# Performance work log

Hardware: AMD Instinct MI355X
Metric: run time of the kernel (lower is better)

The kernel has to match this reference:

```python
import jax, jax.numpy as jnp
import numpy as np

N, IN_F, OUT_F = 65536, 512, 512


def setup_inputs() -> dict:
    key = jax.random.key(0)
    k1, k2, k3 = jax.random.split(key, 3)
    # Activations arrive as dequant-pending uint8-valued floats in [0, 256).
    x = jax.random.randint(k1, (N, IN_F), 0, 256).astype(jnp.float32)
    weight = jax.random.randint(k2, (OUT_F, IN_F), 0, 256).astype(jnp.int32)
    bias = jax.random.randint(k3, (OUT_F,), -512, 512).astype(jnp.int32)
    return {
        "x": x,
        "weight": weight,
        "bias": bias,
        "M": jnp.asarray(0.0123, dtype=jnp.float32),
        "x_zero": jnp.asarray(128.0, dtype=jnp.float32),
        "w_zero": jnp.asarray(128.0, dtype=jnp.float32),
        "y_zero": jnp.asarray(128.0, dtype=jnp.float32),
    }


def reference(x, weight, bias, M, x_zero, w_zero, y_zero):
    # y = round(linear(x - x_zero, w - w_zero, b) * M + y_zero)
    xs = x - x_zero                                   # [N, IN_F]
    w = weight.astype(jnp.float32) - w_zero           # [OUT_F, IN_F]
    y = jnp.einsum("ni,oi->no", xs, w) + bias.astype(jnp.float32)
    return jnp.round(y * M + y_zero)
```

## Files before the change

### kernel.cpp

```cpp
#include <hip/hip_runtime.h>


#define K_DIM 512
#define OUTF  512
#define NT    8

typedef __attribute__((ext_vector_type(4))) int   i32x4;
typedef __attribute__((ext_vector_type(4))) float f32x4;
typedef __attribute__((ext_vector_type(2))) unsigned int u32x2;

__global__ void wprep(const int* __restrict__ W, unsigned int* __restrict__ Wb,
                      const float* __restrict__ wzp) {
    const int wz = __float2int_rn(wzp[0]);
    int idx = (blockIdx.x * blockDim.x + threadIdx.x) * 4;
    i32x4 w = *reinterpret_cast<const i32x4*>(W + idx);
    unsigned int p = ((unsigned int)(w[0] - wz) & 0xffu)
                   | (((unsigned int)(w[1] - wz) & 0xffu) << 8)
                   | (((unsigned int)(w[2] - wz) & 0xffu) << 16)
                   | (((unsigned int)(w[3] - wz) & 0xffu) << 24);
    Wb[idx >> 2] = p;
}

__global__ __launch_bounds__(512, 4)
void qgemm(const float* __restrict__ X,
           const unsigned char* __restrict__ Wb,
           const int* __restrict__ bias,
           const float* __restrict__ Mp,
           const float* __restrict__ xzp,
           const float* __restrict__ yzp,
           float* __restrict__ Y) {
    __shared__ unsigned char lds[2][4096];

    const int tid  = threadIdx.x;
    const int lane = tid & 63;
    const int wid  = tid >> 6;
    const int fr   = lane & 15;
    const int fq   = lane >> 4;

    const int row0 = blockIdx.x * 64;
    const int c0   = wid * 64;

    const float xzf = xzp[0];

    const int srow = tid >> 3;
    const int sk   = (tid & 7) * 8;
    const float* xbase = X + (size_t)(row0 + srow) * K_DIM + sk;
    const int ldst = (srow >> 4) * 1024 + ((srow & 15) + ((sk >> 4) << 4)) * 16 + (sk & 8);

    f32x4 ra[2][2];

    auto stageA = [&](int t, int s) {
        const float* p = xbase + t * 64;
        ra[s][0] = *reinterpret_cast<const f32x4*>(p);
        ra[s][1] = *reinterpret_cast<const f32x4*>(p + 4);
    };
    auto convwrite = [&](int buf, int s) {
        u32x2 v;
        #pragma unroll
        for (int h = 0; h < 2; ++h) {
            unsigned int u0 = (unsigned int)((int)(ra[s][h][0] - xzf)) & 0xffu;
            unsigned int u1 = (unsigned int)((int)(ra[s][h][1] - xzf)) & 0xffu;
            unsigned int u2 = (unsigned int)((int)(ra[s][h][2] - xzf)) & 0xffu;
            unsigned int u3 = (unsigned int)((int)(ra[s][h][3] - xzf)) & 0xffu;
            v[h] = u0 | (u1 << 8) | (u2 << 16) | (u3 << 24);
        }
        *reinterpret_cast<u32x2*>(&lds[buf][ldst]) = v;
    };

    i32x4 acc[4][4];
    #pragma unroll
    for (int n = 0; n < 4; ++n) {
        const int bv = bias[c0 + n * 16 + fr];
        #pragma unroll
        for (int m = 0; m < 4; ++m)
            acc[m][n] = i32x4{bv, bv, bv, bv};
    }

    const unsigned char* wbb = Wb + (size_t)(c0 + fr) * K_DIM + fq * 16;

    auto compute = [&](int buf, int ks) {
        i32x4 af[4], bf[4];
        #pragma unroll
        for (int m = 0; m < 4; ++m)
            af[m] = *reinterpret_cast<const i32x4*>(&lds[buf][m * 1024 + lane * 16]);
        #pragma unroll
        for (int n = 0; n < 4; ++n)
            bf[n] = *reinterpret_cast<const i32x4*>(wbb + (size_t)n * 16 * K_DIM + ks * 64);
        #pragma unroll
        for (int m = 0; m < 4; ++m)
            #pragma unroll
            for (int n = 0; n < 4; ++n)
                acc[m][n] = __builtin_amdgcn_mfma_i32_16x16x64_i8(
                    af[m], bf[n], acc[m][n], 0, 0, 0);
    };

    auto barrier = [&]() {
        asm volatile("s_waitcnt lgkmcnt(0)" ::: "memory");
        __builtin_amdgcn_s_barrier();
    };

    stageA(0, 0);
    stageA(1, 1);
    convwrite(0, 0);
    barrier();

    #pragma unroll
    for (int t = 0; t < NT; ++t) {
        if (t + 2 < NT) stageA(t + 2, t & 1);
        compute(t & 1, t);
        if (t + 1 < NT) convwrite((t + 1) & 1, (t + 1) & 1);
        barrier();
    }

    const float Mv = Mp[0], yz = yzp[0];
    #pragma unroll
    for (int n = 0; n < 4; ++n) {
        const int col = c0 + n * 16 + fr;
        #pragma unroll
        for (int m = 0; m < 4; ++m) {
            const int row = row0 + m * 16 + fq * 4;
            float* yp = Y + (size_t)row * OUTF + col;
            #pragma unroll
            for (int j = 0; j < 4; ++j)
                yp[(size_t)j * OUTF] = rintf((float)acc[m][n][j] * Mv + yz);
        }
    }
}

extern "C" void kernel_launch(void* const* d_in, const int* in_sizes, int n_in,
                              void* d_out, int out_size, void* d_ws, size_t ws_size,
                              hipStream_t stream) {
    const float* x    = (const float*)d_in[0];
    const int*   w    = (const int*)d_in[1];
    const int*   bias = (const int*)d_in[2];
    const float* M    = (const float*)d_in[3];
    const float* xz   = (const float*)d_in[4];
    const float* wz   = (const float*)d_in[5];
    const float* yz   = (const float*)d_in[6];
    float* y = (float*)d_out;

    unsigned int* Wb = (unsigned int*)d_ws;

    wprep<<<256, 256, 0, stream>>>(w, Wb, wz);
    qgemm<<<1024, 512, 0, stream>>>(x, (const unsigned char*)Wb, bias, M, xz, yz, y);
}
```

Baseline: 78.66 us.

## Warp-specialize qgemm into producer/consumer waves with 128x128 tiles and triple buffering

Splits each block into four producer waves and four MFMA consumer waves. The producers convert fp32 X to int8 into LDS and bring weights in with global_load_lds, while the consumers compute from a three-stage LDS ring. Tiles change from 64 rows by all 512 columns to 128x128, with an XCD-aware block remap so the four column tiles of a row band land on the same L2. The aim is to overlap conversion and loads with MFMA work and to serve weights from LDS. The cost is that each X row band is now fetched by four blocks, which adds global or L2 traffic on what is already a bandwidth-bound fp32 input, and half the waves no longer issue MFMAs.

Result: slower. 101.3 us (+28.7%).

```diff
diff --git a/kernel.cpp b/kernel.cpp
--- a/kernel.cpp
+++ b/kernel.cpp
@@ -7,7 +7,12 @@
 
 typedef __attribute__((ext_vector_type(4))) int   i32x4;
 typedef __attribute__((ext_vector_type(4))) float f32x4;
-typedef __attribute__((ext_vector_type(2))) unsigned int u32x2;
+
+__device__ __forceinline__ void gload16(const void* g, void* l) {
+    __builtin_amdgcn_global_load_lds(
+        (const __attribute__((address_space(1))) void*)g,
+        (__attribute__((address_space(3))) void*)l, 16, 0, 0);
+}
 
 __global__ void wprep(const int* __restrict__ W, unsigned int* __restrict__ Wb,
                       const float* __restrict__ wzp) {
@@ -29,100 +34,128 @@
            const float* __restrict__ xzp,
            const float* __restrict__ yzp,
            float* __restrict__ Y) {
-    __shared__ unsigned char lds[2][4096];
+    __shared__ unsigned char lds[3][16384];
 
     const int tid  = threadIdx.x;
     const int lane = tid & 63;
     const int wid  = tid >> 6;
-    const int fr   = lane & 15;
-    const int fq   = lane >> 4;
 
-    const int row0 = blockIdx.x * 64;
-    const int c0   = wid * 64;
+    const int b = blockIdx.x;
+    const int lid = (b & 7) * 256 + (b >> 3);
+    const int row0 = (lid >> 2) * 128;
+    const int n0   = (lid & 3) * 128;
 
-    const float xzf = xzp[0];
+    if (wid < 4) {
+        const float xzf = xzp[0];
+        const int j = tid;
+        const int r = j >> 1;
+        const int mfrag = r >> 4;
+        const int dA = mfrag * 1024 + ((r & 15) + 32 * (j & 1)) * 16;
+        const float* xbase = X + (size_t)(row0 + r) * K_DIM + (j & 1) * 32;
+        const unsigned char* wbase =
+            Wb + (size_t)(n0 + wid * 32 + (lane & 15)) * K_DIM + (lane >> 4) * 16;
 
-    const int srow = tid >> 3;
-    const int sk   = (tid & 7) * 8;
-    const float* xbase = X + (size_t)(row0 + srow) * K_DIM + sk;
-    const int ldst = (srow >> 4) * 1024 + ((srow & 15) + ((sk >> 4) << 4)) * 16 + (sk & 8);
+        f32x4 ra[2][8];
 
-    f32x4 ra[2][2];
+        auto stageA = [&](int tt) {
+            const float* p = xbase + tt * 64;
+            #pragma unroll
+            for (int q = 0; q < 8; ++q)
+                ra[tt & 1][q] = *reinterpret_cast<const f32x4*>(p + q * 4);
+        };
+        auto gloadB = [&](int tt) {
+            unsigned char* base = &lds[tt % 3][8192 + (2 * wid) * 1024];
+            const unsigned char* g = wbase + tt * 64;
+            gload16(g,              base);
+            gload16(g + 16 * K_DIM, base + 1024);
+        };
+        auto convwrite = [&](int tt) {
+            int pk[8];
+            #pragma unroll
+            for (int w = 0; w < 8; ++w) {
+                const f32x4 v = ra[tt & 1][w];
+                unsigned int u0 = (unsigned int)((int)(v[0] - xzf)) & 0xffu;
+                unsigned int u1 = (unsigned int)((int)(v[1] - xzf)) & 0xffu;
+                unsigned int u2 = (unsigned int)((int)(v[2] - xzf)) & 0xffu;
+                unsigned int u3 = (unsigned int)((int)(v[3] - xzf)) & 0xffu;
+                pk[w] = (int)(u0 | (u1 << 8) | (u2 << 16) | (u3 << 24));
+            }
+            unsigned char* base = &lds[tt % 3][dA];
+            *reinterpret_cast<i32x4*>(base)       = i32x4{pk[0], pk[1], pk[2], pk[3]};
+            *reinterpret_cast<i32x4*>(base + 256) = i32x4{pk[4], pk[5], pk[6], pk[7]};
+        };
 
-    auto stageA = [&](int t, int s) {
-        const float* p = xbase + t * 64;
-        ra[s][0] = *reinterpret_cast<const f32x4*>(p);
-        ra[s][1] = *reinterpret_cast<const f32x4*>(p + 4);
-    };
-    auto convwrite = [&](int buf, int s) {
-        u32x2 v;
+        stageA(0); gloadB(0); stageA(1); gloadB(1);
+        convwrite(0);
+        __builtin_amdgcn_sched_barrier(0);
+        asm volatile("s_waitcnt vmcnt(10) lgkmcnt(0)" ::: "memory");
+        __builtin_amdgcn_s_barrier();
+
         #pragma unroll
-        for (int h = 0; h < 2; ++h) {
-            unsigned int u0 = (unsigned int)((int)(ra[s][h][0] - xzf)) & 0xffu;
-            unsigned int u1 = (unsigned int)((int)(ra[s][h][1] - xzf)) & 0xffu;
-            unsigned int u2 = (unsigned int)((int)(ra[s][h][2] - xzf)) & 0xffu;
-            unsigned int u3 = (unsigned int)((int)(ra[s][h][3] - xzf)) & 0xffu;
-            v[h] = u0 | (u1 << 8) | (u2 << 16) | (u3 << 24);
+        for (int t = 0; t < NT - 2; ++t) {
+            stageA(t + 2);
+            gloadB(t + 2);
+            convwrite(t + 1);
+            __builtin_amdgcn_sched_barrier(0);
+            asm volatile("s_waitcnt vmcnt(10) lgkmcnt(0)" ::: "memory");
+            __builtin_amdgcn_s_barrier();
         }
-        *reinterpret_cast<u32x2*>(&lds[buf][ldst]) = v;
-    };
+        convwrite(NT - 1);
+        __builtin_amdgcn_sched_barrier(0);
+        asm volatile("s_waitcnt vmcnt(0) lgkmcnt(0)" ::: "memory");
+        __builtin_amdgcn_s_barrier();
+        __builtin_amdgcn_s_barrier();
+    } else {
+        const int q4 = wid - 4;
+        const int wr = q4 >> 1;
+        const int wc = q4 & 1;
+        const int fr = lane & 15;
+        const int fq = lane >> 4;
 
-    i32x4 acc[4][4];
-    #pragma unroll
-    for (int n = 0; n < 4; ++n) {
-        const int bv = bias[c0 + n * 16 + fr];
+        i32x4 acc[4][4];
         #pragma unroll
-        for (int m = 0; m < 4; ++m)
-            acc[m][n] = i32x4{bv, bv, bv, bv};
-    }
+        for (int n = 0; n < 4; ++n) {
+            const int bv = bias[n0 + wc * 64 + n * 16 + fr];
+            #pragma unroll
+            for (int m = 0; m < 4; ++m)
+                acc[m][n] = i32x4{bv, bv, bv, bv};
+        }
 
-    const unsigned char* wbb = Wb + (size_t)(c0 + fr) * K_DIM + fq * 16;
+        __builtin_amdgcn_s_barrier();
 
-    auto compute = [&](int buf, int ks) {
-        i32x4 af[4], bf[4];
         #pragma unroll
-        for (int m = 0; m < 4; ++m)
-            af[m] = *reinterpret_cast<const i32x4*>(&lds[buf][m * 1024 + lane * 16]);
-        #pragma unroll
-        for (int n = 0; n < 4; ++n)
-            bf[n] = *reinterpret_cast<const i32x4*>(wbb + (size_t)n * 16 * K_DIM + ks * 64);
-        #pragma unroll
-        for (int m = 0; m < 4; ++m)
+        for (int t = 0; t < NT; ++t) {
+            const int bb = t % 3;
+            i32x4 af[4], bf[4];
+            #pragma unroll
+            for (int m = 0; m < 4; ++m)
+                af[m] = *reinterpret_cast<const i32x4*>(
+                    &lds[bb][(wr * 4 + m) * 1024 + lane * 16]);
             #pragma unroll
             for (int n = 0; n < 4; ++n)
-                acc[m][n] = __builtin_amdgcn_mfma_i32_16x16x64_i8(
-                    af[m], bf[n], acc[m][n], 0, 0, 0);
-    };
+                bf[n] = *reinterpret_cast<const i32x4*>(
+                    &lds[bb][8192 + (wc * 4 + n) * 1024 + lane * 16]);
+            #pragma unroll
+            for (int m = 0; m < 4; ++m)
+                #pragma unroll
+                for (int n = 0; n < 4; ++n)
+                    acc[m][n] = __builtin_amdgcn_mfma_i32_16x16x64_i8(
+                        af[m], bf[n], acc[m][n], 0, 0, 0);
+            __builtin_amdgcn_s_barrier();
+        }
 
-    auto barrier = [&]() {
-        asm volatile("s_waitcnt lgkmcnt(0)" ::: "memory");
-        __builtin_amdgcn_s_barrier();
-    };
-
-    stageA(0, 0);
-    stageA(1, 1);
-    convwrite(0, 0);
-    barrier();
-
-    #pragma unroll
-    for (int t = 0; t < NT; ++t) {
-        if (t + 2 < NT) stageA(t + 2, t & 1);
-        compute(t & 1, t);
-        if (t + 1 < NT) convwrite((t + 1) & 1, (t + 1) & 1);
-        barrier();
-    }
-
-    const float Mv = Mp[0], yz = yzp[0];
-    #pragma unroll
-    for (int n = 0; n < 4; ++n) {
-        const int col = c0 + n * 16 + fr;
+        const float Mv = Mp[0], yz = yzp[0];
         #pragma unroll
-        for (int m = 0; m < 4; ++m) {
-            const int row = row0 + m * 16 + fq * 4;
-            float* yp = Y + (size_t)row * OUTF + col;
+        for (int n = 0; n < 4; ++n) {
+            const int col = n0 + wc * 64 + n * 16 + fr;
             #pragma unroll
-            for (int j = 0; j < 4; ++j)
-                yp[(size_t)j * OUTF] = rintf((float)acc[m][n][j] * Mv + yz);
+            for (int m = 0; m < 4; ++m) {
+                const int row = row0 + wr * 64 + m * 16 + fq * 4;
+                float* yp = Y + (size_t)row * OUTF + col;
+                #pragma unroll
+                for (int jj = 0; jj < 4; ++jj)
+                    yp[(size_t)jj * OUTF] = rintf((float)acc[m][n][jj] * Mv + yz);
+            }
         }
     }
 }
@@ -142,5 +175,5 @@
     unsigned int* Wb = (unsigned int*)d_ws;
 
     wprep<<<256, 256, 0, stream>>>(w, Wb, wz);
-    qgemm<<<1024, 512, 0, stream>>>(x, (const unsigned char*)Wb, bias, M, xz, yz, y);
+    qgemm<<<2048, 512, 0, stream>>>(x, (const unsigned char*)Wb, bias, M, xz, yz, y);
 }
```
